# Kernel optimization log

Hardware: AMD Instinct MI355X
Metric: run time of the kernel (lower is better)

Reference implementation:

```python
import jax, jax.numpy as jnp
import numpy as np

B, T = 64, 256
IN, HID, OUT = 512, 1024, 256
NUM_DOMAINS = 20

def setup_inputs() -> dict:
    key = jax.random.key(0)
    k1, k2, k3, k4 = jax.random.split(key, 4)
    x = jax.random.normal(k1, (B, T, IN), dtype=jnp.float32)
    hetero_info = jax.random.randint(k2, (B, 2), 0, NUM_DOMAINS, dtype=jnp.int64)
    # embedding tables init N(0, 0.02) as in the torch module
    fc1_table = 0.02 * jax.random.normal(k3, (NUM_DOMAINS, IN * HID + HID), dtype=jnp.float32)
    fc2_table = 0.02 * jax.random.normal(k4, (NUM_DOMAINS, HID * OUT + OUT), dtype=jnp.float32)
    return {"x": x, "hetero_info": hetero_info, "fc1_table": fc1_table, "fc2_table": fc2_table}

def reference(x, hetero_info, fc1_table, fc2_table):
    domain_id = hetero_info[:, 0].astype(jnp.int32)
    Bn = domain_id.shape[0]
    fc1_param = fc1_table[domain_id]                     # (B, IN*HID + HID)
    w1 = fc1_param[:, : IN * HID].reshape(Bn, IN, HID)   # (B, IN, HID)
    b1 = fc1_param[:, IN * HID:].reshape(Bn, 1, HID)
    fc2_param = fc2_table[domain_id]                     # (B, HID*OUT + OUT)
    w2 = fc2_param[:, : HID * OUT].reshape(Bn, HID, OUT) # (B, HID, OUT)
    b2 = fc2_param[:, HID * OUT:].reshape(Bn, 1, OUT)
    h = jnp.einsum('bti,bih->bth', x, w1) + b1
    h = jax.nn.gelu(h, approximate=False)  # torch nn.GELU default = exact erf
    out = jnp.einsum('bth,bho->bto', h, w2) + b2
    return out
```

## Files before the change

### kernel.cpp

```cpp
#include <hip/hip_runtime.h>
#include <math.h>

#define B_  64
#define T_  256
#define IN_ 512
#define HID_ 1024
#define OUT_ 256
#define NDOM 20

typedef __bf16 bf16_t;
typedef __bf16 bf16x8 __attribute__((ext_vector_type(8)));
typedef __bf16 bf16x4 __attribute__((ext_vector_type(4)));
typedef float  f32x4  __attribute__((ext_vector_type(4)));

__device__ __forceinline__ unsigned f2bf_bits(float f) {
    unsigned u = __builtin_bit_cast(unsigned, f);
    return (u + 0x7FFFu + ((u >> 16) & 1u)) >> 16;
}
__device__ __forceinline__ unsigned pack_bf16x2(float x, float y) {
    return f2bf_bits(x) | (f2bf_bits(y) << 16);
}

__device__ __forceinline__ void gl_lds16(const void* g, void* l) {
    __builtin_amdgcn_global_load_lds(
        (const __attribute__((address_space(1))) unsigned*)g,
        (__attribute__((address_space(3))) unsigned*)l,
        16, 0, 0);
}

__device__ __forceinline__ float gelu_fast(float v) {
    const float t = v * 0.70710678118654752f;
    const float a = __builtin_fabsf(t);
    const float k = __builtin_amdgcn_rcpf(__builtin_fmaf(0.3275911f, a, 1.0f));
    float p = __builtin_fmaf(1.061405429f, k, -1.453152027f);
    p = __builtin_fmaf(p, k, 1.421413741f);
    p = __builtin_fmaf(p, k, -0.284496736f);
    p = __builtin_fmaf(p, k, 0.254829592f);
    p = p * k;
    const float e  = __expf(-a * a);
    const float er = __builtin_fmaf(-p, e, 1.0f);
    const float erf_t = __builtin_copysignf(er, t);
    return 0.5f * v * (1.0f + erf_t);
}

__global__ __launch_bounds__(256) void cvt_x(
    const float* __restrict__ X, bf16_t* __restrict__ Xbf)
{
    const size_t idx = (size_t)blockIdx.x * 256 + threadIdx.x;
    float4 v = ((const float4*)X)[idx];
    uint2 p;
    p.x = pack_bf16x2(v.x, v.y);
    p.y = pack_bf16x2(v.z, v.w);
    ((uint2*)Xbf)[idx] = p;
}

template<int K, int N>
__global__ __launch_bounds__(256) void cvt_transpose(
    const float* __restrict__ table, bf16_t* __restrict__ Wt, float* __restrict__ BiasOut)
{
    const int d  = blockIdx.z;
    const float* W = table + (size_t)d * ((size_t)K * N + N);
    const int n0 = blockIdx.x * 64;
    const int k0 = blockIdx.y * 64;
    const int tid = threadIdx.x;

    __shared__ float t[64][65];

    #pragma unroll
    for (int r = 0; r < 4; ++r) {
        const int kl = (tid >> 4) + r * 16;
        const int nl = (tid & 15) * 4;
        float4 v = *(const float4*)(W + (size_t)(k0 + kl) * N + n0 + nl);
        t[kl][nl + 0] = v.x; t[kl][nl + 1] = v.y;
        t[kl][nl + 2] = v.z; t[kl][nl + 3] = v.w;
    }
    __syncthreads();

    bf16_t* Wtd = Wt + (size_t)d * K * N;
    #pragma unroll
    for (int r = 0; r < 4; ++r) {
        const int nl = (tid >> 4) + r * 16;
        const int k4 = (tid & 15) * 4;
        uint2 p;
        p.x = pack_bf16x2(t[k4 + 0][nl], t[k4 + 1][nl]);
        p.y = pack_bf16x2(t[k4 + 2][nl], t[k4 + 3][nl]);
        *(uint2*)(Wtd + (size_t)(n0 + nl) * K + k0 + k4) = p;
    }

    if (blockIdx.y == 0 && tid < 64)
        BiasOut[(size_t)d * N + n0 + tid] = W[(size_t)K * N + n0 + tid];
}

#define CT_STRIDE 136
__global__ __launch_bounds__(256) void fc1_gemm(
    const bf16_t* __restrict__ Xbf,
    const bf16_t* __restrict__ W1t,
    const float*  __restrict__ Bias,
    const int*    __restrict__ hetero,
    bf16_t*       __restrict__ H)
{
    const int id   = blockIdx.x;
    const int g    = id & 127;
    const int nidx = id >> 7;
    const int b    = g >> 1;
    const int m0   = (g & 1) * 128;
    const int n0   = nidx * 128;
    const int d    = hetero[2 * b];
    const bf16_t* W    = W1t + (size_t)d * HID_ * IN_;
    const float*  bias = Bias + (size_t)d * HID_;
    const bf16_t* A    = Xbf + (size_t)(b * 256 + m0) * IN_;

    __shared__ __attribute__((aligned(16))) char smem[34816];

    const int tid  = threadIdx.x;
    const int wave = tid >> 6;
    const int lane = tid & 63;
    const int l16  = lane & 15;
    const int quad = lane >> 4;
    const int wm   = (wave >> 1) * 64;
    const int wn   = (wave & 1) * 64;

    f32x4 acc[4][4] = {};

    auto ldsA = [&](int nb) -> bf16_t* { return (bf16_t*)(smem + nb * 16384); };
    auto ldsB = [&](int nb) -> bf16_t* { return (bf16_t*)(smem + 8192 + nb * 16384); };

    auto stageA = [&](int kk, bf16_t* dst) {
        #pragma unroll
        for (int cc = 0; cc < 2; ++cc) {
            const int r0  = wave * 32 + cc * 16;
            const int row = r0 + (lane >> 2);
            const int cs  = (lane & 3) ^ ((row >> 1) & 3);
            gl_lds16(A + (size_t)row * IN_ + kk + cs * 8, dst + r0 * 32);
        }
    };
    auto stageB = [&](int kk, bf16_t* dst) {
        #pragma unroll
        for (int cc = 0; cc < 2; ++cc) {
            const int r0  = wave * 32 + cc * 16;
            const int row = r0 + (lane >> 2);
            const int cs  = (lane & 3) ^ ((row >> 1) & 3);
            gl_lds16(W + (size_t)(n0 + row) * IN_ + kk + cs * 8, dst + r0 * 32);
        }
    };
    auto compute = [&](const bf16_t* La, const bf16_t* Lb) {
        bf16x8 af[4], bfg[4];
        #pragma unroll
        for (int i = 0; i < 4; ++i) {
            const int r = wm + i * 16 + l16;
            const int c = quad ^ ((r >> 1) & 3);
            af[i] = *(const bf16x8*)&La[r * 32 + c * 8];
        }
        #pragma unroll
        for (int j = 0; j < 4; ++j) {
            const int r = wn + j * 16 + l16;
            const int c = quad ^ ((r >> 1) & 3);
            bfg[j] = *(const bf16x8*)&Lb[r * 32 + c * 8];
        }
        #pragma unroll
        for (int i = 0; i < 4; ++i)
            #pragma unroll
            for (int j = 0; j < 4; ++j)
                acc[i][j] = __builtin_amdgcn_mfma_f32_16x16x32_bf16(bfg[j], af[i], acc[i][j], 0, 0, 0);
    };

    stageA(0, ldsA(0));
    stageB(0, ldsB(0));
    __syncthreads();

    int buf = 0;
    for (int s = 0; s < 15; ++s) {
        stageA((s + 1) * 32, ldsA(buf ^ 1));
        stageB((s + 1) * 32, ldsB(buf ^ 1));
        compute(ldsA(buf), ldsB(buf));
        __syncthreads();
        buf ^= 1;
    }
    compute(ldsA(buf), ldsB(buf));
    __syncthreads();

    bf16_t* Ct = (bf16_t*)smem;

    #pragma unroll
    for (int i = 0; i < 4; ++i) {
        const int m = wm + i * 16 + l16;
        #pragma unroll
        for (int j = 0; j < 4; ++j) {
            const int nl = wn + j * 16 + quad * 4;
            const float4 b4 = *(const float4*)&bias[n0 + nl];
            bf16x4 w;
            w[0] = (bf16_t)gelu_fast(acc[i][j][0] + b4.x);
            w[1] = (bf16_t)gelu_fast(acc[i][j][1] + b4.y);
            w[2] = (bf16_t)gelu_fast(acc[i][j][2] + b4.z);
            w[3] = (bf16_t)gelu_fast(acc[i][j][3] + b4.w);
            *(bf16x4*)&Ct[m * CT_STRIDE + nl] = w;
        }
    }
    __syncthreads();

    #pragma unroll
    for (int it = 0; it < 8; ++it) {
        const int row = it * 16 + (tid >> 4);
        const int ch  = tid & 15;
        uint4 v = *(const uint4*)&Ct[row * CT_STRIDE + ch * 8];
        *(uint4*)&H[((size_t)(b * 256 + m0 + row)) * HID_ + n0 + ch * 8] = v;
    }
}

__global__ __launch_bounds__(256) void fc2_gemm(
    const bf16_t* __restrict__ H,
    const bf16_t* __restrict__ W2t,
    const float*  __restrict__ Bias,
    const int*    __restrict__ hetero,
    float*        __restrict__ Out)
{
    const int id   = blockIdx.x;
    const int g    = id & 255;
    const int nidx = id >> 8;
    const int b    = g >> 2;
    const int m0   = (g & 3) * 64;
    const int n0   = nidx * 128;
    const int d    = hetero[2 * b];
    const bf16_t* W    = W2t + (size_t)d * OUT_ * HID_;
    const float*  bias = Bias + (size_t)d * OUT_;
    const bf16_t* A    = H + (size_t)(b * 256 + m0) * HID_;

    __shared__ __attribute__((aligned(16))) char smem[49152];

    const int tid  = threadIdx.x;
    const int wave = tid >> 6;
    const int lane = tid & 63;
    const int l16  = lane & 15;
    const int quad = lane >> 4;
    const int wm   = (wave >> 1) * 32;
    const int wn   = (wave & 1) * 64;

    f32x4 acc[2][4] = {};

    auto ldsA = [&](int nb) -> bf16_t* { return (bf16_t*)(smem + nb * 24576); };
    auto ldsB = [&](int nb) -> bf16_t* { return (bf16_t*)(smem + 8192 + nb * 24576); };

    auto stage = [&](int kk, int nb) {
        bf16_t* dA = ldsA(nb);
        bf16_t* dB = ldsB(nb);
        #pragma unroll
        for (int cc = 0; cc < 2; ++cc) {
            const int r0  = wave * 16 + cc * 8;
            const int row = r0 + (lane >> 3);
            const int cs  = (lane & 7) ^ (row & 7);
            gl_lds16(A + (size_t)row * HID_ + kk + cs * 8, dA + r0 * 64);
        }
        #pragma unroll
        for (int cc = 0; cc < 4; ++cc) {
            const int r0  = wave * 32 + cc * 8;
            const int row = r0 + (lane >> 3);
            const int cs  = (lane & 7) ^ (row & 7);
            gl_lds16(W + (size_t)(n0 + row) * HID_ + kk + cs * 8, dB + r0 * 64);
        }
    };
    auto compute = [&](int nb) {
        const bf16_t* La = ldsA(nb);
        const bf16_t* Lb = ldsB(nb);
        #pragma unroll
        for (int h = 0; h < 2; ++h) {
            bf16x8 af[2], bfg[4];
            #pragma unroll
            for (int i = 0; i < 2; ++i) {
                const int r = wm + i * 16 + l16;
                const int c = (h * 4 + quad) ^ (r & 7);
                af[i] = *(const bf16x8*)&La[r * 64 + c * 8];
            }
            #pragma unroll
            for (int j = 0; j < 4; ++j) {
                const int r = wn + j * 16 + l16;
                const int c = (h * 4 + quad) ^ (r & 7);
                bfg[j] = *(const bf16x8*)&Lb[r * 64 + c * 8];
            }
            #pragma unroll
            for (int i = 0; i < 2; ++i)
                #pragma unroll
                for (int j = 0; j < 4; ++j)
                    acc[i][j] = __builtin_amdgcn_mfma_f32_16x16x32_bf16(bfg[j], af[i], acc[i][j], 0, 0, 0);
        }
    };

    stage(0, 0);
    __syncthreads();
    int buf = 0;
    for (int s = 0; s < 15; ++s) {
        stage((s + 1) * 64, buf ^ 1);
        compute(buf);
        __syncthreads();
        buf ^= 1;
    }
    compute(buf);

    #pragma unroll
    for (int i = 0; i < 2; ++i) {
        const int m = m0 + wm + i * 16 + l16;
        #pragma unroll
        for (int j = 0; j < 4; ++j) {
            const int nl = wn + j * 16 + quad * 4;
            const float4 b4 = *(const float4*)&bias[n0 + nl];
            float4 o;
            o.x = acc[i][j][0] + b4.x;
            o.y = acc[i][j][1] + b4.y;
            o.z = acc[i][j][2] + b4.z;
            o.w = acc[i][j][3] + b4.w;
            *(float4*)&Out[(size_t)(b * 256 + m) * OUT_ + n0 + nl] = o;
        }
    }
}

extern "C" void kernel_launch(void* const* d_in, const int* in_sizes, int n_in,
                              void* d_out, int out_size, void* d_ws, size_t ws_size,
                              hipStream_t stream) {
    const float* x         = (const float*)d_in[0];
    const int*   hetero    = (const int*)d_in[1];
    const float* fc1_table = (const float*)d_in[2];
    const float* fc2_table = (const float*)d_in[3];
    float*       out       = (float*)d_out;

    char* ws = (char*)d_ws;
    bf16_t* W1t = (bf16_t*)(ws);
    bf16_t* W2t = (bf16_t*)(ws + 20971520);
    float*  b1  = (float*)(ws + 31457280);
    float*  b2  = (float*)(ws + 31539200);
    bf16_t* H   = (bf16_t*)(ws + 31559680);

    bf16_t* Xbf = (bf16_t*)d_out;

    cvt_x<<<dim3(8192), 256, 0, stream>>>(x, Xbf);
    cvt_transpose<IN_, HID_><<<dim3(HID_ / 64, IN_ / 64, NDOM), 256, 0, stream>>>(
        fc1_table, W1t, b1);
    cvt_transpose<HID_, OUT_><<<dim3(OUT_ / 64, HID_ / 64, NDOM), 256, 0, stream>>>(
        fc2_table, W2t, b2);

    fc1_gemm<<<dim3(1024), 256, 0, stream>>>(Xbf, W1t, b1, hetero, H);
    fc2_gemm<<<dim3(512), 256, 0, stream>>>(H, W2t, b2, hetero, out);
}
```

Baseline: 184.8 us.

## Fuse x conversion into fc1 GEMM and merge weight conversion kernels

Removes the separate fp32-to-bf16 conversion kernel for x. The fc1 GEMM now loads fp32 x tiles into registers, converts them, and writes them to LDS after the MFMA compute step, replacing the direct global-to-LDS loads. The two weight transpose-convert launches are merged into one kernel that uses a flat block index. This saves launches and a full round trip of x through memory, at the cost of extra registers and VALU conversion work inside the GEMM main loop.

```diff
diff --git a/kernel.cpp b/kernel.cpp
--- a/kernel.cpp
+++ b/kernel.cpp
@@ -43,26 +43,26 @@
     return 0.5f * v * (1.0f + erf_t);
 }
 
-__global__ __launch_bounds__(256) void cvt_x(
-    const float* __restrict__ X, bf16_t* __restrict__ Xbf)
+__global__ __launch_bounds__(256) void cvt_weights(
+    const float* __restrict__ T1, const float* __restrict__ T2,
+    bf16_t* __restrict__ W1t, bf16_t* __restrict__ W2t,
+    float* __restrict__ b1, float* __restrict__ b2)
 {
-    const size_t idx = (size_t)blockIdx.x * 256 + threadIdx.x;
-    float4 v = ((const float4*)X)[idx];
-    uint2 p;
-    p.x = pack_bf16x2(v.x, v.y);
-    p.y = pack_bf16x2(v.z, v.w);
-    ((uint2*)Xbf)[idx] = p;
-}
-
-template<int K, int N>
-__global__ __launch_bounds__(256) void cvt_transpose(
-    const float* __restrict__ table, bf16_t* __restrict__ Wt, float* __restrict__ BiasOut)
-{
-    const int d  = blockIdx.z;
+    const int tid = threadIdx.x;
+    int blk = blockIdx.x;
+    const float* table; bf16_t* Wt; float* Bias;
+    int K, N, d, n0, k0;
+    if (blk < 2560) {
+        d = blk >> 7; const int rem = blk & 127;
+        k0 = (rem >> 4) * 64; n0 = (rem & 15) * 64;
+        K = 512; N = 1024; table = T1; Wt = W1t; Bias = b1;
+    } else {
+        blk -= 2560;
+        d = blk >> 6; const int rem = blk & 63;
+        k0 = (rem >> 2) * 64; n0 = (rem & 3) * 64;
+        K = 1024; N = 256; table = T2; Wt = W2t; Bias = b2;
+    }
     const float* W = table + (size_t)d * ((size_t)K * N + N);
-    const int n0 = blockIdx.x * 64;
-    const int k0 = blockIdx.y * 64;
-    const int tid = threadIdx.x;
 
     __shared__ float t[64][65];
 
@@ -87,13 +87,13 @@
         *(uint2*)(Wtd + (size_t)(n0 + nl) * K + k0 + k4) = p;
     }
 
-    if (blockIdx.y == 0 && tid < 64)
-        BiasOut[(size_t)d * N + n0 + tid] = W[(size_t)K * N + n0 + tid];
+    if (k0 == 0 && tid < 64)
+        Bias[(size_t)d * N + n0 + tid] = W[(size_t)K * N + n0 + tid];
 }
 
 #define CT_STRIDE 136
 __global__ __launch_bounds__(256) void fc1_gemm(
-    const bf16_t* __restrict__ Xbf,
+    const float*  __restrict__ X,
     const bf16_t* __restrict__ W1t,
     const float*  __restrict__ Bias,
     const int*    __restrict__ hetero,
@@ -108,7 +108,7 @@
     const int d    = hetero[2 * b];
     const bf16_t* W    = W1t + (size_t)d * HID_ * IN_;
     const float*  bias = Bias + (size_t)d * HID_;
-    const bf16_t* A    = Xbf + (size_t)(b * 256 + m0) * IN_;
+    const float*  A    = X + (size_t)(b * 256 + m0) * IN_;
 
     __shared__ __attribute__((aligned(16))) char smem[34816];
 
@@ -120,18 +120,34 @@
     const int wm   = (wave >> 1) * 64;
     const int wn   = (wave & 1) * 64;
 
+    const int ar = tid >> 2;
+    const int ap = tid & 3;
+
     f32x4 acc[4][4] = {};
+    float4 pre[2][2];
 
     auto ldsA = [&](int nb) -> bf16_t* { return (bf16_t*)(smem + nb * 16384); };
     auto ldsB = [&](int nb) -> bf16_t* { return (bf16_t*)(smem + 8192 + nb * 16384); };
 
-    auto stageA = [&](int kk, bf16_t* dst) {
-        #pragma unroll
-        for (int cc = 0; cc < 2; ++cc) {
-            const int r0  = wave * 32 + cc * 16;
-            const int row = r0 + (lane >> 2);
-            const int cs  = (lane & 3) ^ ((row >> 1) & 3);
-            gl_lds16(A + (size_t)row * IN_ + kk + cs * 8, dst + r0 * 32);
+    auto loadA = [&](int kk) {
+        #pragma unroll
+        for (int r = 0; r < 2; ++r) {
+            const float* src = A + (size_t)(ar + 64 * r) * IN_ + kk + ap * 8;
+            pre[r][0] = *(const float4*)src;
+            pre[r][1] = *(const float4*)(src + 4);
+        }
+    };
+    auto writeA = [&](bf16_t* dst) {
+        #pragma unroll
+        for (int r = 0; r < 2; ++r) {
+            const int row = ar + 64 * r;
+            const int cs  = ap ^ ((row >> 1) & 3);
+            bf16x8 w;
+            w[0] = (bf16_t)pre[r][0].x; w[1] = (bf16_t)pre[r][0].y;
+            w[2] = (bf16_t)pre[r][0].z; w[3] = (bf16_t)pre[r][0].w;
+            w[4] = (bf16_t)pre[r][1].x; w[5] = (bf16_t)pre[r][1].y;
+            w[6] = (bf16_t)pre[r][1].z; w[7] = (bf16_t)pre[r][1].w;
+            *(bf16x8*)&dst[row * 32 + cs * 8] = w;
         }
     };
     auto stageB = [&](int kk, bf16_t* dst) {
@@ -164,15 +180,17 @@
                 acc[i][j] = __builtin_amdgcn_mfma_f32_16x16x32_bf16(bfg[j], af[i], acc[i][j], 0, 0, 0);
     };
 
-    stageA(0, ldsA(0));
+    loadA(0);
     stageB(0, ldsB(0));
+    writeA(ldsA(0));
     __syncthreads();
 
     int buf = 0;
     for (int s = 0; s < 15; ++s) {
-        stageA((s + 1) * 32, ldsA(buf ^ 1));
+        loadA((s + 1) * 32);
         stageB((s + 1) * 32, ldsB(buf ^ 1));
         compute(ldsA(buf), ldsB(buf));
+        writeA(ldsA(buf ^ 1));
         __syncthreads();
         buf ^= 1;
     }
@@ -328,14 +346,7 @@
     float*  b2  = (float*)(ws + 31539200);
     bf16_t* H   = (bf16_t*)(ws + 31559680);
 
-    bf16_t* Xbf = (bf16_t*)d_out;
-
-    cvt_x<<<dim3(8192), 256, 0, stream>>>(x, Xbf);
-    cvt_transpose<IN_, HID_><<<dim3(HID_ / 64, IN_ / 64, NDOM), 256, 0, stream>>>(
-        fc1_table, W1t, b1);
-    cvt_transpose<HID_, OUT_><<<dim3(OUT_ / 64, HID_ / 64, NDOM), 256, 0, stream>>>(
-        fc2_table, W2t, b2);
-
-    fc1_gemm<<<dim3(1024), 256, 0, stream>>>(Xbf, W1t, b1, hetero, H);
+    cvt_weights<<<dim3(3840), 256, 0, stream>>>(fc1_table, fc2_table, W1t, W2t, b1, b2);
+    fc1_gemm<<<dim3(1024), 256, 0, stream>>>(x, W1t, b1, hetero, H);
     fc2_gemm<<<dim3(512), 256, 0, stream>>>(H, W2t, b2, hetero, out);
 }
```

Measured after the change: 178.6 us. 1.04x faster.
